# Kernel optimization log

Hardware: AMD Instinct MI355X
Metric: run time of the kernel (lower is better)

The kernel has to match this reference:

```python
import jax, jax.numpy as jnp
import numpy as np

B, N, D = 2, 2048, 1024
H, HD = 16, 64
BASE = 10000.0
INIT_STD = 0.02


def apply_rope(x, base=BASE):
    """Rotary embedding on the last dim; seq axis is axis 1.

    Works for q of shape (b, n, h, d) and k of shape (b, n, d).
    """
    d = x.shape[-1]
    n = x.shape[1]
    half = d // 2
    inv_freq = 1.0 / (base ** (jnp.arange(half, dtype=jnp.float32) / half))
    ang = jnp.arange(n, dtype=jnp.float32)[:, None] * inv_freq  # (n, d/2)
    extra = x.ndim - 3  # axes between seq axis and feature axis
    ang = ang.reshape((n,) + (1,) * extra + (half,))
    cos, sin = jnp.cos(ang), jnp.sin(ang)
    x1, x2 = jnp.split(x, 2, axis=-1)
    return jnp.concatenate([x1 * cos - x2 * sin, x2 * cos + x1 * sin], axis=-1)


def setup_inputs() -> dict:
    key = jax.random.key(0)
    kx, k1, k2, k3, k4 = jax.random.split(key, 5)
    x = jax.random.normal(kx, (B, N, D), dtype=jnp.float32)
    Wq = jax.random.normal(k1, (D, H * HD), dtype=jnp.float32) * INIT_STD
    Wkv = jax.random.normal(k2, (D, 2 * HD), dtype=jnp.float32) * INIT_STD
    Wkvh = jax.random.normal(k3, (D, 2 * H), dtype=jnp.float32) * INIT_STD
    Wo = jax.random.normal(k4, (H * HD, D), dtype=jnp.float32) * INIT_STD
    return {"x": x, "Wq": Wq, "Wkv": Wkv, "Wkvh": Wkvh, "Wo": Wo}


def reference(x, Wq, Wkv, Wkvh, Wo):
    b, n, d = x.shape
    q = (x @ Wq).reshape(b, n, H, HD)          # (b,n,h,hd)
    kv = x @ Wkv                                # (b,n,2*hd)
    kv_head = jax.nn.sigmoid(x @ Wkvh)          # (b,n,2*h)
    k, v = jnp.split(kv, 2, axis=-1)            # each (b,n,hd)
    k_head, v_head = jnp.split(kv_head, 2, axis=-1)  # each (b,n,h)

    # LRPE (rotary) on q and on the shared low-rank k
    q = apply_rope(q)
    k = apply_rope(k)

    # outer-product expansion: (b,n,h) x (b,n,hd) -> (b,n,h,hd)
    k = jnp.einsum('bnh,bnd->bnhd', k_head, k)
    v = jnp.einsum('bnh,bnd->bnhd', v_head, v)

    # causal softmax attention, scale = 1/sqrt(head_dim)
    scale = 1.0 / np.sqrt(HD)
    scores = jnp.einsum('bqhd,bkhd->bhqk', q, k) * scale
    mask = jnp.tril(jnp.ones((n, n), dtype=bool))
    scores = jnp.where(mask, scores, jnp.finfo(scores.dtype).min)
    p = jax.nn.softmax(scores, axis=-1)
    out = jnp.einsum('bhqk,bkhd->bqhd', p, v)   # (b,n,h,hd)

    out = out.reshape(b, n, H * HD)
    return out @ Wo
```

## Files before the change

### kernel.cpp

```cpp
#include <hip/hip_runtime.h>

typedef unsigned short u16;
typedef unsigned int u32;
typedef __attribute__((ext_vector_type(8))) short short8;
typedef __attribute__((ext_vector_type(4))) float f32x4;
typedef __attribute__((ext_vector_type(4))) u32 u32x4;
typedef __attribute__((ext_vector_type(2))) u32 u32x2;
typedef __attribute__((ext_vector_type(4))) u16 u16x4;

constexpr int B_ = 2, N_ = 2048, H_ = 16;
constexpr int ROWS = B_ * N_;
constexpr float LOG2E = 1.44269504088896f;

__device__ __forceinline__ float bf2f(u16 u){ union{u32 u; float f;} v; v.u = ((u32)u)<<16; return v.f; }
__device__ __forceinline__ u16 f2bf(float f){
  union{float f; u32 u;} v; v.f = f;
  u32 u = v.u; u += 0x7fffu + ((u>>16)&1u);
  return (u16)(u>>16);
}
__device__ __forceinline__ u32 cvtpk(float lo, float hi){
  u32 r; asm("v_cvt_pk_bf16_f32 %0, %1, %2" : "=v"(r) : "v"(lo), "v"(hi)); return r;
}

__global__ __launch_bounds__(256) void k_setup(const float* __restrict__ x, u16* __restrict__ xb,
                                               float2* __restrict__ tab,
                                               const float* __restrict__ Wq, const float* __restrict__ Wo,
                                               u16* __restrict__ WqT, u16* __restrict__ WoT,
                                               const float* __restrict__ Wkv, const float* __restrict__ Wkvh,
                                               u16* __restrict__ WkvT){
  __shared__ float T[64*65];
  int bid = blockIdx.x, tid = threadIdx.x;
  if (bid < 4096){
    int i = (bid*256 + tid)*4;
    f32x4 v = *(const f32x4*)(x + i);
    u16x4 o; o[0]=f2bf(v[0]); o[1]=f2bf(v[1]); o[2]=f2bf(v[2]); o[3]=f2bf(v[3]);
    *(u16x4*)(xb + i) = o;
    return;
  }
  if (bid < 4352){
    int idx = (bid-4096)*256 + tid;
    int i = idx & 31, n = idx >> 5;
    float ang = (float)n * exp2f(-(float)i * 0.4152410118609203f);
    tab[idx] = make_float2(cosf(ang), sinf(ang));
    return;
  }
  if (bid < 4864){
    int m = (bid - 4352) >> 8;
    const float* in = m ? Wo : Wq;
    u16* out = m ? WoT : WqT;
    int t2 = (bid - 4352) & 255;
    int n0 = (t2 & 15) << 6, k0 = (t2 >> 4) << 6;
    #pragma unroll
    for (int s=0; s<4; ++s){
      int chunk = tid + s*256, r = chunk >> 4, c4 = (chunk & 15) << 2;
      *(f32x4*)(&T[r*65 + c4]) = *(const f32x4*)(&in[(size_t)(k0 + r)*1024 + n0 + c4]);
    }
    __syncthreads();
    #pragma unroll
    for (int s=0; s<2; ++s){
      int chunk = tid + s*256, d = chunk >> 3, c8 = (chunk & 7) << 3;
      u16x4 o1, o2;
      #pragma unroll
      for (int j=0; j<4; ++j){ o1[j] = f2bf(T[(c8+j)*65 + d]); o2[j] = f2bf(T[(c8+4+j)*65 + d]); }
      *(u16x4*)(&out[(size_t)(n0 + d)*1024 + k0 + c8])     = o1;
      *(u16x4*)(&out[(size_t)(n0 + d)*1024 + k0 + c8 + 4]) = o2;
    }
    return;
  }
  {
    int idx = (bid - 4864)*256 + tid;
    int n = idx >> 10, k = idx & 1023;
    float v = 0.f;
    if (n < 128)      v = Wkv[k*128 + n];
    else if (n < 160) v = Wkvh[k*32 + (n-128)];
    WkvT[idx] = f2bf(v);
  }
}

template<int MODE>
__global__ __launch_bounds__(256) void k_gemm_mn(const u16* __restrict__ A, const u16* __restrict__ Bt,
                                                 void* __restrict__ Cv, float* __restrict__ proj,
                                                 const float2* __restrict__ tab,
                                                 int M, int N, int K){
  __shared__ u16 As[128*64];
  __shared__ u16 Bs[64*64];
  int ntile = N >> 6;
  int m0 = (blockIdx.x / ntile) << 7;
  int n0 = (blockIdx.x % ntile) << 6;
  int tid = threadIdx.x;
  int l = tid & 63, lr = l & 15, lc = l >> 4;
  int w = tid >> 6;
  int wm = w * 32;
  f32x4 acc[2][4] = {};
  for (int kt = 0; kt < K; kt += 64){
    __syncthreads();
    #pragma unroll
    for (int s = 0; s < 4; ++s){
      int chunk = tid + s*256, r = chunk >> 3, c8 = (chunk & 7) << 3;
      __builtin_amdgcn_global_load_lds(
        (const __attribute__((address_space(1))) u32*)(&A[(size_t)(m0 + r)*K + kt + c8]),
        (__attribute__((address_space(3))) u32*)(&As[r*64 + c8]), 16, 0, 0);
    }
    #pragma unroll
    for (int s = 0; s < 2; ++s){
      int chunk = tid + s*256, r = chunk >> 3, c8 = (chunk & 7) << 3;
      __builtin_amdgcn_global_load_lds(
        (const __attribute__((address_space(1))) u32*)(&Bt[(size_t)(n0 + r)*K + kt + c8]),
        (__attribute__((address_space(3))) u32*)(&Bs[r*64 + c8]), 16, 0, 0);
    }
    __syncthreads();
    short8 af[2][2], bfr[4][2];
    #pragma unroll
    for (int m=0; m<2; ++m)
      #pragma unroll
      for (int c=0; c<2; ++c)
        af[m][c] = *(const short8*)(&As[(wm + m*16 + lr)*64 + c*32 + lc*8]);
    #pragma unroll
    for (int n=0; n<4; ++n)
      #pragma unroll
      for (int c=0; c<2; ++c)
        bfr[n][c] = *(const short8*)(&Bs[(n*16 + lr)*64 + c*32 + lc*8]);
    __builtin_amdgcn_s_setprio(1);
    #pragma unroll
    for (int m=0; m<2; ++m)
      #pragma unroll
      for (int n=0; n<4; ++n)
        #pragma unroll
        for (int c=0; c<2; ++c)
          acc[m][n] = __builtin_amdgcn_mfma_f32_16x16x32_bf16(af[m][c], bfr[n][c], acc[m][n], 0,0,0);
    __builtin_amdgcn_s_setprio(0);
  }
  if constexpr (MODE == 0){
    float* C = (float*)Cv;
    #pragma unroll
    for (int m=0; m<2; ++m)
      #pragma unroll
      for (int n=0; n<4; ++n)
        #pragma unroll
        for (int r=0; r<4; ++r)
          C[(size_t)(m0 + wm + m*16 + lc*4 + r)*N + n0 + n*16 + lr] = acc[m][n][r];
  } else {
    if (n0 < 1024){
      u16* C = (u16*)Cv;
      #pragma unroll
      for (int m=0; m<2; ++m){
        int grow = m0 + wm + m*16 + lc*4;
        #pragma unroll
        for (int nf=0; nf<2; ++nf){
          int i = nf*16 + lr;
          #pragma unroll
          for (int r=0; r<4; ++r){
            float2 cs = tab[(size_t)((grow + r) & (N_-1))*32 + i];
            float x1 = acc[m][nf][r], x2 = acc[m][nf+2][r];
            C[(size_t)(grow + r)*1024 + n0 + i]      = f2bf(0.125f*(x1*cs.x - x2*cs.y));
            C[(size_t)(grow + r)*1024 + n0 + i + 32] = f2bf(0.125f*(x2*cs.x + x1*cs.y));
          }
        }
      }
    } else {
      int pc = n0 - 1024;
      #pragma unroll
      for (int m=0; m<2; ++m)
        #pragma unroll
        for (int n=0; n<4; ++n)
          #pragma unroll
          for (int r=0; r<4; ++r)
            proj[(size_t)(m0 + wm + m*16 + lc*4 + r)*192 + pc + n*16 + lr] = acc[m][n][r];
    }
  }
}

__global__ __launch_bounds__(256) void k_postproc2(const float* __restrict__ proj, const float2* __restrict__ tab,
                                                   u16* __restrict__ k_rope, float* __restrict__ k_head,
                                                   float* __restrict__ v_head, u16* __restrict__ vt){
  __shared__ u16 Tv[64*72];
  int n0 = blockIdx.x << 6;
  int b = n0 >> 11;
  int tid = threadIdx.x;
  #pragma unroll
  for (int s=0; s<4; ++s){
    int chunk = tid + s*256, r = chunk >> 4, c4 = (chunk & 15) << 2;
    f32x4 v = *(const f32x4*)(&proj[(size_t)(n0+r)*192 + 64 + c4]);
    u16x4 o; o[0]=f2bf(v[0]); o[1]=f2bf(v[1]); o[2]=f2bf(v[2]); o[3]=f2bf(v[3]);
    *(u16x4*)(&Tv[r*72 + c4]) = o;
  }
  int wv = tid>>6, t = tid&63;
  for (int rr = wv; rr < 64; rr += 4){
    int row = n0 + rr, n = row & (N_-1);
    const float* p = proj + (size_t)row*192;
    if (t < 32){
      float hv = 1.f/(1.f + __expf(-p[128 + t]));
      if (t < 16) k_head[((size_t)b*16 + t)*N_ + n] = hv * LOG2E;
      else        v_head[((size_t)b*16 + (t-16))*N_ + n] = hv;
      float2 cs = tab[n*32 + t];
      float k1 = p[t], k2 = p[32 + t];
      k_rope[(size_t)row*64 + t]      = f2bf(k1*cs.x - k2*cs.y);
      k_rope[(size_t)row*64 + 32 + t] = f2bf(k2*cs.x + k1*cs.y);
    }
  }
  __syncthreads();
  int nb = n0 & (N_-1);
  #pragma unroll
  for (int s=0; s<2; ++s){
    int chunk = tid + s*256, d = chunk>>3, c8 = (chunk&7)<<3;
    u32x4 o; u16* op = (u16*)&o;
    #pragma unroll
    for (int j=0; j<8; ++j) op[j] = Tv[(c8+j)*72 + d];
    *(u32x4*)(&vt[((size_t)b*64 + d)*N_ + nb + c8]) = o;
  }
}

__global__ __launch_bounds__(256, 4) void k_attn7(const u16* __restrict__ q_bf, const u16* __restrict__ k_rp,
                                                  const u16* __restrict__ vt, const float* __restrict__ k_hd,
                                                  const float* __restrict__ v_hd,
                                                  u16* __restrict__ o_part, float* __restrict__ l_part){
  __shared__ u16 Ks[64*72];
  __shared__ u16 Vts[64*72];
  __shared__ u16 Ps[4][16*72];
  __shared__ float g_s[128];
  int z = blockIdx.x;
  int pidx = z >> 1, sp = z & 1;
  int qt = 31 - (pidx >> 5);
  int h = pidx & 15, b = (pidx >> 4) & 1;
  int h0 = (qt + 1) >> 1;
  int t0 = sp ? h0 : 0, t1 = sp ? (qt + 1) : h0;
  int tid = threadIdx.x, w = tid>>6, l = tid&63, lr = l&15, lc = l>>4;
  if (t0 >= t1){
    u16* op = o_part + (size_t)z*4096;
    for (int i = tid; i < 512; i += 256) *(u32x4*)(op + i*8) = (u32x4){0,0,0,0};
    if (tid < 64) l_part[z*64 + tid] = 0.f;
    return;
  }
  size_t rowbase = (size_t)b*N_;
  size_t qoff = (rowbase + qt*64 + w*16 + lr)*1024 + h*64;
  short8 qf0 = *(const short8*)(&q_bf[qoff + lc*8]);
  short8 qf1 = *(const short8*)(&q_bf[qoff + 32 + lc*8]);
  const float* gkp = k_hd + ((size_t)b*16 + h)*N_;
  const float* gvp = v_hd + ((size_t)b*16 + h)*N_;
  u32x4 kr[2], vr[2]; float gr;
  auto issue = [&](int t){
    int kg0 = t << 6;
    #pragma unroll
    for (int s=0; s<2; ++s){
      int chunk = tid + s*256, r = chunk>>3, c8 = (chunk&7)<<3;
      kr[s] = *(const u32x4*)(&k_rp[(rowbase + kg0 + r)*64 + c8]);
      vr[s] = *(const u32x4*)(&vt[((size_t)b*64 + r)*N_ + kg0 + c8]);
    }
    gr = (tid < 64) ? gkp[kg0 + tid] : ((tid < 128) ? gvp[kg0 + tid - 64] : 0.f);
  };
  float lsum = 0.f;
  f32x4 o[4] = {};
  issue(t0);
  for (int t = t0; t < t1; ++t){
    int kg0 = t << 6;
    __syncthreads();
    #pragma unroll
    for (int s=0; s<2; ++s){
      int chunk = tid + s*256, r = chunk>>3, c8 = (chunk&7)<<3;
      *(u32x4*)(&Ks[r*72 + c8])  = kr[s];
      *(u32x4*)(&Vts[r*72 + c8]) = vr[s];
    }
    if (tid < 128) g_s[tid] = gr;
    if (t + 1 < t1) issue(t+1);
    __syncthreads();
    f32x4 s4[4];
    __builtin_amdgcn_s_setprio(1);
    #pragma unroll
    for (int nf=0; nf<4; ++nf){
      short8 kf0 = *(const short8*)(&Ks[(nf*16+lr)*72 + lc*8]);
      short8 kf1 = *(const short8*)(&Ks[(nf*16+lr)*72 + 32 + lc*8]);
      f32x4 zz = {};
      zz = __builtin_amdgcn_mfma_f32_16x16x32_bf16(kf0, qf0, zz, 0,0,0);
      s4[nf] = __builtin_amdgcn_mfma_f32_16x16x32_bf16(kf1, qf1, zz, 0,0,0);
    }
    __builtin_amdgcn_s_setprio(0);
    #pragma unroll
    for (int nf=0; nf<4; ++nf){
      f32x4 gkv = *(const f32x4*)(&g_s[nf*16 + lc*4]);
      #pragma unroll
      for (int r=0; r<4; ++r) s4[nf][r] *= gkv[r];
    }
    if (t == qt){
      int qg = qt*64 + w*16 + lr;
      #pragma unroll
      for (int nf=0; nf<4; ++nf)
        #pragma unroll
        for (int r=0; r<4; ++r)
          if (kg0 + nf*16 + lc*4 + r > qg) s4[nf][r] = -1e30f;
    }
    #pragma unroll
    for (int nf=0; nf<4; ++nf)
      #pragma unroll
      for (int r=0; r<4; ++r){ s4[nf][r] = exp2f(s4[nf][r]); lsum += s4[nf][r]; }
    #pragma unroll
    for (int nf=0; nf<4; ++nf){
      f32x4 gvv = *(const f32x4*)(&g_s[64 + nf*16 + lc*4]);
      u32 lo = cvtpk(s4[nf][0]*gvv[0], s4[nf][1]*gvv[1]);
      u32 hi = cvtpk(s4[nf][2]*gvv[2], s4[nf][3]*gvv[3]);
      *(u32x2*)(&Ps[w][lr*72 + nf*16 + lc*4]) = (u32x2){lo, hi};
    }
    asm volatile("s_waitcnt lgkmcnt(0)" ::: "memory");
    __builtin_amdgcn_sched_barrier(0);
    short8 pf0 = *(const short8*)(&Ps[w][lr*72 + lc*8]);
    short8 pf1 = *(const short8*)(&Ps[w][lr*72 + 32 + lc*8]);
    __builtin_amdgcn_s_setprio(1);
    #pragma unroll
    for (int nf=0; nf<4; ++nf){
      short8 vf0 = *(const short8*)(&Vts[(nf*16+lr)*72 + lc*8]);
      short8 vf1 = *(const short8*)(&Vts[(nf*16+lr)*72 + 32 + lc*8]);
      o[nf] = __builtin_amdgcn_mfma_f32_16x16x32_bf16(pf0, vf0, o[nf], 0,0,0);
      o[nf] = __builtin_amdgcn_mfma_f32_16x16x32_bf16(pf1, vf1, o[nf], 0,0,0);
    }
    __builtin_amdgcn_s_setprio(0);
  }
  lsum += __shfl_xor(lsum, 16);
  lsum += __shfl_xor(lsum, 32);
  if (lc == 0) l_part[z*64 + w*16 + lr] = lsum;
  u16* op = o_part + (size_t)z*4096;
  #pragma unroll
  for (int nf=0; nf<4; ++nf)
    #pragma unroll
    for (int r=0; r<4; ++r)
      op[(w*16 + lc*4 + r)*64 + nf*16 + lr] = f2bf(o[nf][r]);
}

__global__ __launch_bounds__(256) void k_comb(const u16* __restrict__ o_part, const float* __restrict__ l_part,
                                              u16* __restrict__ attn_o){
  int z2 = blockIdx.x;
  int qt = 31 - (z2 >> 5), h = z2 & 15, b = (z2 >> 4) & 1;
  int tid = threadIdx.x;
  int q = tid >> 2, c16 = (tid & 3) << 4;
  size_t base0 = (size_t)(2*z2)*4096 + q*64 + c16;
  float lv = l_part[(2*z2)*64 + q] + l_part[(2*z2+1)*64 + q];
  float rl = __builtin_amdgcn_rcpf(lv);
  union U8 { u32x4 v; u16 s[8]; };
  U8 a0, a1, b0, b1, r0, r1;
  a0.v = *(const u32x4*)(o_part + base0);
  a1.v = *(const u32x4*)(o_part + base0 + 8);
  b0.v = *(const u32x4*)(o_part + base0 + 4096);
  b1.v = *(const u32x4*)(o_part + base0 + 4096 + 8);
  #pragma unroll
  for (int j=0; j<8; ++j){
    r0.s[j] = f2bf((bf2f(a0.s[j]) + bf2f(b0.s[j])) * rl);
    r1.s[j] = f2bf((bf2f(a1.s[j]) + bf2f(b1.s[j])) * rl);
  }
  u16* outp = attn_o + ((size_t)(b*N_ + qt*64 + q))*1024 + h*64 + c16;
  *(u32x4*)outp = r0.v;
  *(u32x4*)(outp + 8) = r1.v;
}

extern "C" void kernel_launch(void* const* d_in, const int* in_sizes, int n_in,
                              void* d_out, int out_size, void* d_ws, size_t ws_size,
                              hipStream_t stream){
  const float* x    = (const float*)d_in[0];
  const float* Wq   = (const float*)d_in[1];
  const float* Wkv  = (const float*)d_in[2];
  const float* Wkvh = (const float*)d_in[3];
  const float* Wo   = (const float*)d_in[4];
  float* out = (float*)d_out;

  char* p = (char*)d_ws;
  u16* xb      = (u16*)p;   p += (size_t)ROWS*1024*2;
  u16* WT      = (u16*)p;   p += (size_t)1216*1024*2;
  u16* WoT     = (u16*)p;   p += (size_t)1024*1024*2;
  float* proj  = (float*)p; p += (size_t)ROWS*192*4;
  u16* q_bf    = (u16*)p;   p += (size_t)ROWS*1024*2;
  u16* k_rp    = (u16*)p;   p += (size_t)ROWS*64*2;
  u16* vt      = (u16*)p;   p += (size_t)B_*64*N_*2;
  float* k_hd  = (float*)p; p += (size_t)B_*H_*N_*4;
  float* v_hd  = (float*)p; p += (size_t)B_*H_*N_*4;
  float2* tab  = (float2*)p; p += (size_t)N_*32*8;
  u16* o_part  = (u16*)p;   p += (size_t)2048*4096*2;
  float* l_part= (float*)p; p += (size_t)2048*64*4;
  u16* attn_o  = xb;

  k_setup<<<4096 + 256 + 512 + 768, 256, 0, stream>>>(x, xb, tab, Wq, Wo, WT, WoT,
                                                      Wkv, Wkvh, WT + (size_t)1024*1024);
  k_gemm_mn<1><<<(ROWS/128)*(1216/64), 256, 0, stream>>>(xb, WT, q_bf, proj, tab, ROWS, 1216, 1024);
  k_postproc2<<<ROWS/64, 256, 0, stream>>>(proj, tab, k_rp, k_hd, v_hd, vt);
  k_attn7<<<2048, 256, 0, stream>>>(q_bf, k_rp, vt, k_hd, v_hd, o_part, l_part);
  k_comb<<<1024, 256, 0, stream>>>(o_part, l_part, attn_o);
  k_gemm_mn<0><<<(ROWS/128)*(1024/64), 256, 0, stream>>>(attn_o, WoT, out, nullptr, nullptr, ROWS, 1024, 1024);
}
```

Measured before the change: 113.9 us.

## Process two heads per attention block to reuse shared K/V tiles

The attention kernel now handles a pair of heads per workgroup. Since K and V are shared across heads (low-rank expansion), each LDS-loaded K/V tile is reused for two heads' QK and PV MFMAs, which halves global K/V traffic and the number of blocks. The combine kernel is remapped to the new partial-output layout. This doubles per-thread accumulator registers under launch_bounds(256,4), so it risks spills or lower occupancy, and the grid drops to 1024 blocks.

```diff
diff --git a/kernel.cpp b/kernel.cpp
--- a/kernel.cpp
+++ b/kernel.cpp
@@ -210,33 +210,38 @@
   }
 }
 
-__global__ __launch_bounds__(256, 4) void k_attn7(const u16* __restrict__ q_bf, const u16* __restrict__ k_rp,
+__global__ __launch_bounds__(256, 4) void k_attn8(const u16* __restrict__ q_bf, const u16* __restrict__ k_rp,
                                                   const u16* __restrict__ vt, const float* __restrict__ k_hd,
                                                   const float* __restrict__ v_hd,
                                                   u16* __restrict__ o_part, float* __restrict__ l_part){
   __shared__ u16 Ks[64*72];
   __shared__ u16 Vts[64*72];
   __shared__ u16 Ps[4][16*72];
-  __shared__ float g_s[128];
+  __shared__ float g_s[256];
   int z = blockIdx.x;
   int pidx = z >> 1, sp = z & 1;
-  int qt = 31 - (pidx >> 5);
-  int h = pidx & 15, b = (pidx >> 4) & 1;
-  int h0 = (qt + 1) >> 1;
-  int t0 = sp ? h0 : 0, t1 = sp ? (qt + 1) : h0;
+  int qt = 31 - (pidx >> 4);
+  int hp = pidx & 7, b = (pidx >> 3) & 1;
+  int h0 = hp*2, h1 = h0 + 1;
+  int half = (qt + 1) >> 1;
+  int t0 = sp ? half : 0, t1 = sp ? (qt + 1) : half;
   int tid = threadIdx.x, w = tid>>6, l = tid&63, lr = l&15, lc = l>>4;
   if (t0 >= t1){
-    u16* op = o_part + (size_t)z*4096;
-    for (int i = tid; i < 512; i += 256) *(u32x4*)(op + i*8) = (u32x4){0,0,0,0};
-    if (tid < 64) l_part[z*64 + tid] = 0.f;
+    u16* op = o_part + (size_t)z*8192;
+    for (int i = tid; i < 1024; i += 256) *(u32x4*)(op + i*8) = (u32x4){0,0,0,0};
+    if (tid < 128) l_part[z*128 + tid] = 0.f;
     return;
   }
   size_t rowbase = (size_t)b*N_;
-  size_t qoff = (rowbase + qt*64 + w*16 + lr)*1024 + h*64;
-  short8 qf0 = *(const short8*)(&q_bf[qoff + lc*8]);
-  short8 qf1 = *(const short8*)(&q_bf[qoff + 32 + lc*8]);
-  const float* gkp = k_hd + ((size_t)b*16 + h)*N_;
-  const float* gvp = v_hd + ((size_t)b*16 + h)*N_;
+  size_t qrow = rowbase + qt*64 + w*16 + lr;
+  short8 qA0 = *(const short8*)(&q_bf[qrow*1024 + h0*64 + lc*8]);
+  short8 qA1 = *(const short8*)(&q_bf[qrow*1024 + h0*64 + 32 + lc*8]);
+  short8 qB0 = *(const short8*)(&q_bf[qrow*1024 + h1*64 + lc*8]);
+  short8 qB1 = *(const short8*)(&q_bf[qrow*1024 + h1*64 + 32 + lc*8]);
+  const float* gkp0 = k_hd + ((size_t)b*16 + h0)*N_;
+  const float* gkp1 = k_hd + ((size_t)b*16 + h1)*N_;
+  const float* gvp0 = v_hd + ((size_t)b*16 + h0)*N_;
+  const float* gvp1 = v_hd + ((size_t)b*16 + h1)*N_;
   u32x4 kr[2], vr[2]; float gr;
   auto issue = [&](int t){
     int kg0 = t << 6;
@@ -246,10 +251,12 @@
       kr[s] = *(const u32x4*)(&k_rp[(rowbase + kg0 + r)*64 + c8]);
       vr[s] = *(const u32x4*)(&vt[((size_t)b*64 + r)*N_ + kg0 + c8]);
     }
-    gr = (tid < 64) ? gkp[kg0 + tid] : ((tid < 128) ? gvp[kg0 + tid - 64] : 0.f);
+    int seg = tid >> 6, off = tid & 63;
+    const float* gp = (seg==0) ? gkp0 : (seg==1) ? gkp1 : (seg==2) ? gvp0 : gvp1;
+    gr = gp[kg0 + off];
   };
-  float lsum = 0.f;
-  f32x4 o[4] = {};
+  float lsum0 = 0.f, lsum1 = 0.f;
+  f32x4 o0[4] = {}, o1[4] = {};
   issue(t0);
   for (int t = t0; t < t1; ++t){
     int kg0 = t << 6;
@@ -260,68 +267,102 @@
       *(u32x4*)(&Ks[r*72 + c8])  = kr[s];
       *(u32x4*)(&Vts[r*72 + c8]) = vr[s];
     }
-    if (tid < 128) g_s[tid] = gr;
+    g_s[tid] = gr;
     if (t + 1 < t1) issue(t+1);
     __syncthreads();
-    f32x4 s4[4];
+    f32x4 s0[4], s1[4];
     __builtin_amdgcn_s_setprio(1);
     #pragma unroll
     for (int nf=0; nf<4; ++nf){
       short8 kf0 = *(const short8*)(&Ks[(nf*16+lr)*72 + lc*8]);
       short8 kf1 = *(const short8*)(&Ks[(nf*16+lr)*72 + 32 + lc*8]);
-      f32x4 zz = {};
-      zz = __builtin_amdgcn_mfma_f32_16x16x32_bf16(kf0, qf0, zz, 0,0,0);
-      s4[nf] = __builtin_amdgcn_mfma_f32_16x16x32_bf16(kf1, qf1, zz, 0,0,0);
+      f32x4 z0 = {};
+      z0 = __builtin_amdgcn_mfma_f32_16x16x32_bf16(kf0, qA0, z0, 0,0,0);
+      s0[nf] = __builtin_amdgcn_mfma_f32_16x16x32_bf16(kf1, qA1, z0, 0,0,0);
+      f32x4 z1 = {};
+      z1 = __builtin_amdgcn_mfma_f32_16x16x32_bf16(kf0, qB0, z1, 0,0,0);
+      s1[nf] = __builtin_amdgcn_mfma_f32_16x16x32_bf16(kf1, qB1, z1, 0,0,0);
     }
     __builtin_amdgcn_s_setprio(0);
+    bool diag = (t == qt);
+    int qg = qt*64 + w*16 + lr;
     #pragma unroll
     for (int nf=0; nf<4; ++nf){
-      f32x4 gkv = *(const f32x4*)(&g_s[nf*16 + lc*4]);
-      #pragma unroll
-      for (int r=0; r<4; ++r) s4[nf][r] *= gkv[r];
-    }
-    if (t == qt){
-      int qg = qt*64 + w*16 + lr;
-      #pragma unroll
-      for (int nf=0; nf<4; ++nf)
-        #pragma unroll
-        for (int r=0; r<4; ++r)
-          if (kg0 + nf*16 + lc*4 + r > qg) s4[nf][r] = -1e30f;
+      f32x4 gk0 = *(const f32x4*)(&g_s[nf*16 + lc*4]);
+      f32x4 gk1 = *(const f32x4*)(&g_s[64 + nf*16 + lc*4]);
+      #pragma unroll
+      for (int r=0; r<4; ++r){
+        bool m = diag && (kg0 + nf*16 + lc*4 + r > qg);
+        s0[nf][r] = m ? -1e30f : s0[nf][r]*gk0[r];
+        s1[nf][r] = m ? -1e30f : s1[nf][r]*gk1[r];
+      }
     }
     #pragma unroll
     for (int nf=0; nf<4; ++nf)
       #pragma unroll
-      for (int r=0; r<4; ++r){ s4[nf][r] = exp2f(s4[nf][r]); lsum += s4[nf][r]; }
+      for (int r=0; r<4; ++r){
+        s0[nf][r] = exp2f(s0[nf][r]); lsum0 += s0[nf][r];
+        s1[nf][r] = exp2f(s1[nf][r]); lsum1 += s1[nf][r];
+      }
     #pragma unroll
     for (int nf=0; nf<4; ++nf){
-      f32x4 gvv = *(const f32x4*)(&g_s[64 + nf*16 + lc*4]);
-      u32 lo = cvtpk(s4[nf][0]*gvv[0], s4[nf][1]*gvv[1]);
-      u32 hi = cvtpk(s4[nf][2]*gvv[2], s4[nf][3]*gvv[3]);
+      f32x4 gv0 = *(const f32x4*)(&g_s[128 + nf*16 + lc*4]);
+      u32 lo = cvtpk(s0[nf][0]*gv0[0], s0[nf][1]*gv0[1]);
+      u32 hi = cvtpk(s0[nf][2]*gv0[2], s0[nf][3]*gv0[3]);
       *(u32x2*)(&Ps[w][lr*72 + nf*16 + lc*4]) = (u32x2){lo, hi};
     }
     asm volatile("s_waitcnt lgkmcnt(0)" ::: "memory");
     __builtin_amdgcn_sched_barrier(0);
-    short8 pf0 = *(const short8*)(&Ps[w][lr*72 + lc*8]);
-    short8 pf1 = *(const short8*)(&Ps[w][lr*72 + 32 + lc*8]);
-    __builtin_amdgcn_s_setprio(1);
+    {
+      short8 pf0 = *(const short8*)(&Ps[w][lr*72 + lc*8]);
+      short8 pf1 = *(const short8*)(&Ps[w][lr*72 + 32 + lc*8]);
+      __builtin_amdgcn_s_setprio(1);
+      #pragma unroll
+      for (int nf=0; nf<4; ++nf){
+        short8 vf0 = *(const short8*)(&Vts[(nf*16+lr)*72 + lc*8]);
+        short8 vf1 = *(const short8*)(&Vts[(nf*16+lr)*72 + 32 + lc*8]);
+        o0[nf] = __builtin_amdgcn_mfma_f32_16x16x32_bf16(pf0, vf0, o0[nf], 0,0,0);
+        o0[nf] = __builtin_amdgcn_mfma_f32_16x16x32_bf16(pf1, vf1, o0[nf], 0,0,0);
+      }
+      __builtin_amdgcn_s_setprio(0);
+    }
     #pragma unroll
     for (int nf=0; nf<4; ++nf){
-      short8 vf0 = *(const short8*)(&Vts[(nf*16+lr)*72 + lc*8]);
-      short8 vf1 = *(const short8*)(&Vts[(nf*16+lr)*72 + 32 + lc*8]);
-      o[nf] = __builtin_amdgcn_mfma_f32_16x16x32_bf16(pf0, vf0, o[nf], 0,0,0);
-      o[nf] = __builtin_amdgcn_mfma_f32_16x16x32_bf16(pf1, vf1, o[nf], 0,0,0);
-    }
-    __builtin_amdgcn_s_setprio(0);
-  }
-  lsum += __shfl_xor(lsum, 16);
-  lsum += __shfl_xor(lsum, 32);
-  if (lc == 0) l_part[z*64 + w*16 + lr] = lsum;
-  u16* op = o_part + (size_t)z*4096;
+      f32x4 gv1 = *(const f32x4*)(&g_s[192 + nf*16 + lc*4]);
+      u32 lo = cvtpk(s1[nf][0]*gv1[0], s1[nf][1]*gv1[1]);
+      u32 hi = cvtpk(s1[nf][2]*gv1[2], s1[nf][3]*gv1[3]);
+      *(u32x2*)(&Ps[w][lr*72 + nf*16 + lc*4]) = (u32x2){lo, hi};
+    }
+    asm volatile("s_waitcnt lgkmcnt(0)" ::: "memory");
+    __builtin_amdgcn_sched_barrier(0);
+    {
+      short8 pf0 = *(const short8*)(&Ps[w][lr*72 + lc*8]);
+      short8 pf1 = *(const short8*)(&Ps[w][lr*72 + 32 + lc*8]);
+      __builtin_amdgcn_s_setprio(1);
+      #pragma unroll
+      for (int nf=0; nf<4; ++nf){
+        short8 vf0 = *(const short8*)(&Vts[(nf*16+lr)*72 + lc*8]);
+        short8 vf1 = *(const short8*)(&Vts[(nf*16+lr)*72 + 32 + lc*8]);
+        o1[nf] = __builtin_amdgcn_mfma_f32_16x16x32_bf16(pf0, vf0, o1[nf], 0,0,0);
+        o1[nf] = __builtin_amdgcn_mfma_f32_16x16x32_bf16(pf1, vf1, o1[nf], 0,0,0);
+      }
+      __builtin_amdgcn_s_setprio(0);
+    }
+  }
+  lsum0 += __shfl_xor(lsum0, 16); lsum0 += __shfl_xor(lsum0, 32);
+  lsum1 += __shfl_xor(lsum1, 16); lsum1 += __shfl_xor(lsum1, 32);
+  if (lc == 0){
+    l_part[z*128 + w*16 + lr]      = lsum0;
+    l_part[z*128 + 64 + w*16 + lr] = lsum1;
+  }
+  u16* op = o_part + (size_t)z*8192;
   #pragma unroll
   for (int nf=0; nf<4; ++nf)
     #pragma unroll
-    for (int r=0; r<4; ++r)
-      op[(w*16 + lc*4 + r)*64 + nf*16 + lr] = f2bf(o[nf][r]);
+    for (int r=0; r<4; ++r){
+      op[(w*16 + lc*4 + r)*64 + nf*16 + lr]        = f2bf(o0[nf][r]);
+      op[4096 + (w*16 + lc*4 + r)*64 + nf*16 + lr] = f2bf(o1[nf][r]);
+    }
 }
 
 __global__ __launch_bounds__(256) void k_comb(const u16* __restrict__ o_part, const float* __restrict__ l_part,
@@ -330,15 +371,17 @@
   int qt = 31 - (z2 >> 5), h = z2 & 15, b = (z2 >> 4) & 1;
   int tid = threadIdx.x;
   int q = tid >> 2, c16 = (tid & 3) << 4;
-  size_t base0 = (size_t)(2*z2)*4096 + q*64 + c16;
-  float lv = l_part[(2*z2)*64 + q] + l_part[(2*z2+1)*64 + q];
+  int pidx = ((31 - qt) << 4) | (b << 3) | (h >> 1);
+  int hs = h & 1;
+  size_t base0 = (size_t)(2*pidx)*8192 + hs*4096 + q*64 + c16;
+  float lv = l_part[(2*pidx)*128 + hs*64 + q] + l_part[(2*pidx+1)*128 + hs*64 + q];
   float rl = __builtin_amdgcn_rcpf(lv);
   union U8 { u32x4 v; u16 s[8]; };
   U8 a0, a1, b0, b1, r0, r1;
   a0.v = *(const u32x4*)(o_part + base0);
   a1.v = *(const u32x4*)(o_part + base0 + 8);
-  b0.v = *(const u32x4*)(o_part + base0 + 4096);
-  b1.v = *(const u32x4*)(o_part + base0 + 4096 + 8);
+  b0.v = *(const u32x4*)(o_part + base0 + 8192);
+  b1.v = *(const u32x4*)(o_part + base0 + 8192 + 8);
   #pragma unroll
   for (int j=0; j<8; ++j){
     r0.s[j] = f2bf((bf2f(a0.s[j]) + bf2f(b0.s[j])) * rl);
@@ -370,15 +413,15 @@
   float* k_hd  = (float*)p; p += (size_t)B_*H_*N_*4;
   float* v_hd  = (float*)p; p += (size_t)B_*H_*N_*4;
   float2* tab  = (float2*)p; p += (size_t)N_*32*8;
-  u16* o_part  = (u16*)p;   p += (size_t)2048*4096*2;
-  float* l_part= (float*)p; p += (size_t)2048*64*4;
+  u16* o_part  = (u16*)p;   p += (size_t)1024*8192*2;
+  float* l_part= (float*)p; p += (size_t)1024*128*4;
   u16* attn_o  = xb;
 
   k_setup<<<4096 + 256 + 512 + 768, 256, 0, stream>>>(x, xb, tab, Wq, Wo, WT, WoT,
                                                       Wkv, Wkvh, WT + (size_t)1024*1024);
   k_gemm_mn<1><<<(ROWS/128)*(1216/64), 256, 0, stream>>>(xb, WT, q_bf, proj, tab, ROWS, 1216, 1024);
   k_postproc2<<<ROWS/64, 256, 0, stream>>>(proj, tab, k_rp, k_hd, v_hd, vt);
-  k_attn7<<<2048, 256, 0, stream>>>(q_bf, k_rp, vt, k_hd, v_hd, o_part, l_part);
+  k_attn8<<<1024, 256, 0, stream>>>(q_bf, k_rp, vt, k_hd, v_hd, o_part, l_part);
   k_comb<<<1024, 256, 0, stream>>>(o_part, l_part, attn_o);
   k_gemm_mn<0><<<(ROWS/128)*(1024/64), 256, 0, stream>>>(attn_o, WoT, out, nullptr, nullptr, ROWS, 1024, 1024);
 }
```

Measured after the change: 162.3 us. 42.5% more time.
